# Kernel optimization log

Measured on AMD Instinct MI355X. Metric: run time of the kernel, lower is better.

## Reference

```python
import jax, jax.numpy as jnp
import numpy as np

EPS = 1e-12


def _l2norm(v):
    return v / (jnp.linalg.norm(v) + EPS)


def _sn(W, u):
    """One-step power-iteration spectral normalization (torch spectral_norm, 1x1 conv weight).
    W: (out, in), u: (out,). u/v are treated as buffers (no grad)."""
    Wm = W.reshape(W.shape[0], -1)
    v = _l2norm(Wm.T @ u)
    u2 = _l2norm(Wm @ v)
    u2 = jax.lax.stop_gradient(u2)
    v = jax.lax.stop_gradient(v)
    sigma = u2 @ (Wm @ v)
    return W / sigma


def _maxpool2(x):
    # 2x2 max pool, stride 2, NCHW
    N, C, H, W = x.shape
    return x.reshape(N, C, H // 2, 2, W // 2, 2).max(axis=(3, 5))


def setup_inputs() -> dict:
    key = jax.random.key(0)
    ks = jax.random.split(key, 10)
    N, C, H, W = 16, 256, 64, 64
    s = 0.05  # keep logits moderate
    return {
        "x": jax.random.normal(ks[0], (N, C, H, W), dtype=jnp.float32),
        "Wt": jax.random.normal(ks[1], (C >> 3, C), dtype=jnp.float32) * s,
        "Wp": jax.random.normal(ks[2], (C >> 3, C), dtype=jnp.float32) * s,
        "Wg": jax.random.normal(ks[3], (C >> 1, C), dtype=jnp.float32) * s,
        "Wo": jax.random.normal(ks[4], (C, C >> 1), dtype=jnp.float32) * s,
        "ut": jax.random.normal(ks[5], (C >> 3,), dtype=jnp.float32),
        "up": jax.random.normal(ks[6], (C >> 3,), dtype=jnp.float32),
        "ug": jax.random.normal(ks[7], (C >> 1,), dtype=jnp.float32),
        "uo": jax.random.normal(ks[8], (C,), dtype=jnp.float32),
        "gamma": jnp.float32(0.1),  # nonzero so attention branch is exercised
    }


def reference(x, Wt, Wp, Wg, Wo, ut, up, ug, uo, gamma):
    N, C, H, W = x.shape
    L = H * W          # location_num
    Ld = L // 4        # downsampled_num
    # 1x1 convs as channel einsums with spectrally-normalized weights
    theta = jnp.einsum('oc,nchw->nohw', _sn(Wt, ut), x).reshape(N, C >> 3, L)
    phi = _maxpool2(jnp.einsum('oc,nchw->nohw', _sn(Wp, up), x)).reshape(N, C >> 3, Ld)
    attn = jax.nn.softmax(jnp.einsum('ncl,ncm->nlm', theta, phi), axis=-1)  # (N, L, Ld)
    g = _maxpool2(jnp.einsum('oc,nchw->nohw', _sn(Wg, ug), x)).reshape(N, C >> 1, Ld)
    attn_g = jnp.einsum('ncm,nlm->ncl', g, attn).reshape(N, C >> 1, H, W)
    attn_g = jnp.einsum('oc,nchw->nohw', _sn(Wo, uo), attn_g)
    return x + gamma * attn_g
```

## Files before the change

kernel.cpp:

```cpp
#include <hip/hip_runtime.h>
#include <math.h>

#define EPS 1e-12f

typedef unsigned short ushort_t;
typedef __attribute__((ext_vector_type(8))) short short8;
typedef __attribute__((ext_vector_type(4))) float f32x4;
typedef __attribute__((ext_vector_type(4))) unsigned short ushort4v;
typedef __attribute__((ext_vector_type(2))) unsigned int uint2v;
typedef __attribute__((ext_vector_type(4))) unsigned int uint32x4;

#define WS_WB_F 0
#define WS_WO_F 24576
#define WS_TH_F 40960
#define WS_PH_F 1089536
#define WS_G_F  1351680

__device__ __forceinline__ ushort_t f2bf(float f) {
  unsigned int u = __float_as_uint(f);
  u += 0x7fffu + ((u >> 16) & 1u);
  return (ushort_t)(u >> 16);
}
__device__ __forceinline__ float bf2f(ushort_t u) {
  return __uint_as_float(((unsigned int)u) << 16);
}
__device__ __forceinline__ unsigned int pack_bfrh(float lo, float hi) {
  unsigned int a = __float_as_uint(lo) + 0x8000u;
  unsigned int b = __float_as_uint(hi) + 0x8000u;
  return (a >> 16) | (b & 0xffff0000u);
}
__device__ __forceinline__ float exp2_hw(float x) {
  float r;
  asm("v_exp_f32 %0, %1" : "=v"(r) : "v"(x));
  return r;
}

__device__ __forceinline__ void gload_lds16(const ushort_t* g, ushort_t* l) {
  __builtin_amdgcn_global_load_lds(
      (const __attribute__((address_space(1))) unsigned int*)g,
      (__attribute__((address_space(3))) unsigned int*)l, 16, 0, 0);
}

__device__ __forceinline__ float block_reduce_sum(float v, float* red) {
  int t = threadIdx.x;
  red[t] = v;
  __syncthreads();
  #pragma unroll
  for (int s = 128; s > 0; s >>= 1) {
    if (t < s) red[t] += red[t + s];
    __syncthreads();
  }
  float r = red[0];
  __syncthreads();
  return r;
}

__global__ __launch_bounds__(256) void sn_kernel(
    const float* __restrict__ Wt, const float* __restrict__ Wp,
    const float* __restrict__ Wg, const float* __restrict__ Wo,
    const float* __restrict__ ut, const float* __restrict__ up,
    const float* __restrict__ ug, const float* __restrict__ uo,
    float* __restrict__ ws) {
  __shared__ float red[256];
  __shared__ float ub[256];
  __shared__ float vb[256];
  const float* W; const float* u; int O, Ci;
  switch (blockIdx.x) {
    case 0:  W = Wt; u = ut; O = 32;  Ci = 256; break;
    case 1:  W = Wp; u = up; O = 32;  Ci = 256; break;
    case 2:  W = Wg; u = ug; O = 128; Ci = 256; break;
    default: W = Wo; u = uo; O = 256; Ci = 128; break;
  }
  int t = threadIdx.x;
  if (t < O) ub[t] = u[t];
  __syncthreads();
  float tv = 0.f;
  if (t < Ci) {
    for (int o = 0; o < O; o++) tv += W[o * Ci + t] * ub[o];
  }
  float nt2 = block_reduce_sum((t < Ci) ? tv * tv : 0.f, red);
  float ntn = sqrtf(nt2);
  if (t < Ci) vb[t] = tv / (ntn + EPS);
  __syncthreads();
  float sv = 0.f;
  if (t < O) {
    const float* Wr = W + (size_t)t * Ci;
    for (int c = 0; c < Ci; c += 4) {
      float4 wv = *(const float4*)(Wr + c);
      sv += wv.x * vb[c] + wv.y * vb[c + 1] + wv.z * vb[c + 2] + wv.w * vb[c + 3];
    }
  }
  float ss = block_reduce_sum((t < O) ? sv * sv : 0.f, red);
  float ns = sqrtf(ss);
  float sigma = ss / (ns + EPS);
  float inv = 1.f / sigma;
  if (blockIdx.x == 0) inv *= 1.44269504088896f;
  int total = O * Ci;
  if (blockIdx.x == 3) {
    ushort_t* dst = (ushort_t*)(ws + WS_WO_F);
    for (int i = t; i < total; i += 256) {
      int o = i >> 7, c = i & 127;
      int oct = o >> 4, l16o = o & 15, kc = c >> 5, cl = c & 31;
      int kap = (cl < 16) ? ((cl >> 2) * 8 + (cl & 3))
                          : (((cl >> 2) & 3) * 8 + 4 + (cl & 3));
      dst[(((kc * 16 + oct) * 64 + (kap >> 3) * 16 + l16o) << 3) + (kap & 7)] =
          f2bf(W[i] * inv);
    }
  } else {
    int base_row = (blockIdx.x == 0) ? 0 : (blockIdx.x == 1 ? 32 : 64);
    ushort_t* dst = (ushort_t*)(ws + WS_WB_F);
    for (int i = t; i < total; i += 256) {
      int o = i >> 8, c = i & 255;
      int og = base_row + o;
      int mtg = og >> 4, l16o = og & 15, kc = c >> 5, qd = (c >> 3) & 3, j = c & 7;
      dst[(((mtg * 8 + kc) * 64 + qd * 16 + l16o) << 3) + j] = f2bf(W[i] * inv);
    }
  }
}

__global__ __launch_bounds__(256, 2) void proj_mfma(
    const float* __restrict__ x, const ushort_t* __restrict__ wb,
    ushort_t* __restrict__ theta_b, ushort_t* __restrict__ phi_b,
    ushort_t* __restrict__ g_fb) {
  __shared__ ushort_t xb[128 * 264];
  const int t = threadIdx.x;
  const int n = blockIdx.y;
  const int l0 = blockIdx.x * 128;
  const float* xn = x + ((size_t)n * 256) * 4096 + l0;
  {
    const int lrel = t & 127;
    const int half = t >> 7;
    #pragma unroll 4
    for (int ch = 0; ch < 16; ++ch) {
      int chunk = half * 16 + ch;
      short8 v;
      #pragma unroll
      for (int j = 0; j < 8; ++j) {
        float f = xn[(size_t)(chunk * 8 + j) * 4096 + lrel];
        v[j] = (short)f2bf(f);
      }
      *(short8*)(&xb[lrel * 264 + chunk * 8]) = v;
    }
  }
  __syncthreads();
  const int w = t >> 6;
  const int lane = t & 63;
  const int quad = lane >> 4;
  const int l16 = lane & 15;
  const int rowA = (w * 16 + l16) * 264;
  const int rowB = (64 + w * 16 + l16) * 264;
  const int hd = blockIdx.x;
  #pragma unroll 1
  for (int pass = 0; pass < 2; ++pass) {
    f32x4 accA[6], accB[6];
    #pragma unroll
    for (int i = 0; i < 6; ++i) {
      accA[i] = (f32x4){0.f, 0.f, 0.f, 0.f};
      accB[i] = (f32x4){0.f, 0.f, 0.f, 0.f};
    }
    #pragma unroll
    for (int kc = 0; kc < 8; ++kc) {
      short8 bA = *(const short8*)(&xb[rowA + kc * 32 + quad * 8]);
      short8 bB = *(const short8*)(&xb[rowB + kc * 32 + quad * 8]);
      #pragma unroll
      for (int mt = 0; mt < 6; ++mt) {
        int mtg = pass * 6 + mt;
        short8 aW = *(const short8*)(wb + (((size_t)(mtg * 8 + kc) * 64 + lane) << 3));
        accA[mt] = __builtin_amdgcn_mfma_f32_16x16x32_bf16(aW, bA, accA[mt], 0, 0, 0);
        accB[mt] = __builtin_amdgcn_mfma_f32_16x16x32_bf16(aW, bB, accB[mt], 0, 0, 0);
      }
    }
    #pragma unroll
    for (int mt = 0; mt < 6; ++mt) {
      int mtg = pass * 6 + mt;
      if (mtg < 2) {
        int lA = l0 + w * 16 + l16;
        ushort4v vA, vB;
        #pragma unroll
        for (int r = 0; r < 4; ++r) { vA[r] = f2bf(accA[mt][r]); vB[r] = f2bf(accB[mt][r]); }
        *(ushort4v*)(theta_b + ((size_t)n * 4096 + lA) * 32 + mtg * 16 + quad * 4) = vA;
        *(ushort4v*)(theta_b + ((size_t)n * 4096 + lA + 64) * 32 + mtg * 16 + quad * 4) = vB;
      } else {
        float pm[4];
        #pragma unroll
        for (int r = 0; r < 4; ++r) {
          float v = fmaxf(accA[mt][r], accB[mt][r]);
          v = fmaxf(v, __shfl_xor(v, 1));
          pm[r] = v;
        }
        if ((l16 & 1) == 0) {
          int rr = l16 >> 1;
          if (mtg < 4) {
            int mp = hd * 32 + ((rr & 4) ? 16 : 0) + w * 4 + (rr & 3);
            ushort4v vv;
            #pragma unroll
            for (int r = 0; r < 4; ++r) vv[r] = f2bf(pm[r]);
            *(ushort4v*)(phi_b + ((size_t)n * 1024 + mp) * 32 + (mtg - 2) * 16 + quad * 4) = vv;
          } else {
            size_t fb = (size_t)n * 131072 +
                        (size_t)((hd * 8 + (mtg - 4)) * 64 + w * 16 + quad * 4) * 8 + rr;
            #pragma unroll
            for (int r = 0; r < 4; ++r)
              g_fb[fb + (size_t)r * 8] = f2bf(pm[r]);
          }
        }
      }
    }
  }
}

__global__ __launch_bounds__(256, 4) void attn_mfma(
    const float* __restrict__ x,
    const ushort_t* __restrict__ theta_b,
    const ushort_t* __restrict__ phi_b,
    const ushort_t* __restrict__ g_fb,
    const ushort_t* __restrict__ Wo_fb,
    const float* __restrict__ gamma_p,
    float* __restrict__ out) {
  __shared__ __align__(16) unsigned char smem[34816];
  ushort_t* gbuf = (ushort_t*)smem;
  ushort_t* outb = (ushort_t*)smem;

  const int t = threadIdx.x;
  const int w = t >> 6;
  const int lane = t & 63;
  const int quad = lane >> 4;
  const int l16 = lane & 15;

  const int flat = blockIdx.y * 64 + blockIdx.x;
  const int nf = ((flat & 7) << 7) | (flat >> 3);
  const int n = nf >> 6;
  const int l0 = (nf & 63) << 6;
  const int lq = l0 + w * 16;

  const short8 bth = *(const short8*)(theta_b + ((size_t)n * 4096 + lq + l16) * 32 + quad * 8);
  const ushort_t* phiN = phi_b + (size_t)n * 1024 * 32;
  const ushort_t* gN   = g_fb + (size_t)n * 131072;

  f32x4 oacc[8];
  #pragma unroll
  for (int j = 0; j < 8; ++j) oacc[j] = (f32x4){0.f, 0.f, 0.f, 0.f};
  float M = -3.0e38f, L = 0.f;
  unsigned int pk[16];

  auto STAGE = [&](int mc) {
    const ushort_t* src = gN + (size_t)mc * 16384 + w * 8 * 512 + lane * 8;
    ushort_t* dst = gbuf + w * 8 * 512;
    #pragma unroll
    for (int b = 0; b < 8; ++b)
      gload_lds16(src + b * 512, dst + b * 512);
  };

  auto QKSM = [&](int mc) {
    const int m0 = mc * 128;
    const f32x4 z = (f32x4){0.f, 0.f, 0.f, 0.f};
    f32x4 st[8];
    #pragma unroll
    for (int i = 0; i < 8; ++i) {
      short8 aph = *(const short8*)(phiN + (size_t)(m0 + i * 16 + l16) * 32 + quad * 8);
      st[i] = __builtin_amdgcn_mfma_f32_16x16x32_bf16(aph, bth, z, 0, 0, 0);
    }
    f32x4 a0 = st[0], a1 = st[1], a2 = st[2], a3 = st[3];
    #pragma unroll
    for (int r = 0; r < 4; ++r) {
      a0[r] = fmaxf(a0[r], st[4][r]); a1[r] = fmaxf(a1[r], st[5][r]);
      a2[r] = fmaxf(a2[r], st[6][r]); a3[r] = fmaxf(a3[r], st[7][r]);
    }
    #pragma unroll
    for (int r = 0; r < 4; ++r) { a0[r] = fmaxf(a0[r], a2[r]); a1[r] = fmaxf(a1[r], a3[r]); }
    float mlane = fmaxf(fmaxf(fmaxf(a0[0], a1[0]), fmaxf(a0[1], a1[1])),
                        fmaxf(fmaxf(a0[2], a1[2]), fmaxf(a0[3], a1[3])));
    if (!__all(mlane <= M + 8.0f)) {
      float mx = fmaxf(mlane, __shfl_xor(mlane, 16));
      mx = fmaxf(mx, __shfl_xor(mx, 32));
      float nm = fmaxf(M, mx);
      float al = exp2_hw(M - nm);
      M = nm;
      L *= al;
      #pragma unroll
      for (int j = 0; j < 8; ++j) {
        #pragma unroll
        for (int r = 0; r < 4; ++r) oacc[j][r] *= al;
      }
    }
    #pragma unroll
    for (int i = 0; i < 8; ++i) {
      #pragma unroll
      for (int r = 0; r < 4; ++r) st[i][r] = exp2_hw(st[i][r] - M);
    }
    f32x4 s0 = st[0], s1 = st[1];
    #pragma unroll
    for (int r = 0; r < 4; ++r) {
      s0[r] += st[2][r] + st[4][r] + st[6][r];
      s1[r] += st[3][r] + st[5][r] + st[7][r];
    }
    L += (s0[0] + s1[0]) + (s0[1] + s1[1]) + (s0[2] + s1[2]) + (s0[3] + s1[3]);
    #pragma unroll
    for (int i = 0; i < 8; ++i) {
      pk[2 * i]     = pack_bfrh(st[i][0], st[i][1]);
      pk[2 * i + 1] = pack_bfrh(st[i][2], st[i][3]);
    }
  };

  auto PV = [&]() {
    __builtin_amdgcn_s_setprio(1);
    #pragma unroll
    for (int s = 0; s < 4; ++s) {
      uint32x4 u = {pk[4 * s], pk[4 * s + 1], pk[4 * s + 2], pk[4 * s + 3]};
      short8 pb = __builtin_bit_cast(short8, u);
      #pragma unroll
      for (int j = 0; j < 8; ++j) {
        short8 gf = *(const short8*)(gbuf + (size_t)(s * 8 + j) * 512 + lane * 8);
        oacc[j] = __builtin_amdgcn_mfma_f32_16x16x32_bf16(gf, pb, oacc[j], 0, 0, 0);
      }
    }
    __builtin_amdgcn_s_setprio(0);
  };

  STAGE(0);
  QKSM(0);
  __syncthreads();
  #pragma unroll 1
  for (int mc = 0; mc < 8; ++mc) {
    PV();
    if (mc < 7) {
      __syncthreads();
      STAGE(mc + 1);
      QKSM(mc + 1);
      __syncthreads();
    }
  }
  __syncthreads();

  L += __shfl_xor(L, 16);
  L += __shfl_xor(L, 32);
  const float invL = 1.f / L;

  f32x4 acc2[16];
  #pragma unroll
  for (int i = 0; i < 16; ++i) acc2[i] = (f32x4){0.f, 0.f, 0.f, 0.f};

  short8 aO0, aO1, aO2, aO3;
  {
    uint32x4 u;
    u[0] = pack_bfrh(oacc[0][0] * invL, oacc[0][1] * invL);
    u[1] = pack_bfrh(oacc[0][2] * invL, oacc[0][3] * invL);
    u[2] = pack_bfrh(oacc[1][0] * invL, oacc[1][1] * invL);
    u[3] = pack_bfrh(oacc[1][2] * invL, oacc[1][3] * invL);
    aO0 = __builtin_bit_cast(short8, u);
    u[0] = pack_bfrh(oacc[2][0] * invL, oacc[2][1] * invL);
    u[1] = pack_bfrh(oacc[2][2] * invL, oacc[2][3] * invL);
    u[2] = pack_bfrh(oacc[3][0] * invL, oacc[3][1] * invL);
    u[3] = pack_bfrh(oacc[3][2] * invL, oacc[3][3] * invL);
    aO1 = __builtin_bit_cast(short8, u);
    u[0] = pack_bfrh(oacc[4][0] * invL, oacc[4][1] * invL);
    u[1] = pack_bfrh(oacc[4][2] * invL, oacc[4][3] * invL);
    u[2] = pack_bfrh(oacc[5][0] * invL, oacc[5][1] * invL);
    u[3] = pack_bfrh(oacc[5][2] * invL, oacc[5][3] * invL);
    aO2 = __builtin_bit_cast(short8, u);
    u[0] = pack_bfrh(oacc[6][0] * invL, oacc[6][1] * invL);
    u[1] = pack_bfrh(oacc[6][2] * invL, oacc[6][3] * invL);
    u[2] = pack_bfrh(oacc[7][0] * invL, oacc[7][1] * invL);
    u[3] = pack_bfrh(oacc[7][2] * invL, oacc[7][3] * invL);
    aO3 = __builtin_bit_cast(short8, u);
  }

  {
    const ushort_t* src = Wo_fb + w * 8 * 512 + lane * 8;
    ushort_t* dst = gbuf + w * 8 * 512;
    #pragma unroll
    for (int b = 0; b < 8; ++b)
      gload_lds16(src + b * 512, dst + b * 512);
  }
  __syncthreads();
  #pragma unroll
  for (int oct = 0; oct < 16; ++oct) {
    short8 bw0 = *(const short8*)(gbuf + (size_t)oct * 512 + lane * 8);
    short8 bw1 = *(const short8*)(gbuf + (size_t)(16 + oct) * 512 + lane * 8);
    acc2[oct] = __builtin_amdgcn_mfma_f32_16x16x32_bf16(aO0, bw0, acc2[oct], 0, 0, 0);
    acc2[oct] = __builtin_amdgcn_mfma_f32_16x16x32_bf16(aO1, bw1, acc2[oct], 0, 0, 0);
  }
  __syncthreads();
  {
    const ushort_t* src = Wo_fb + 16384 + w * 8 * 512 + lane * 8;
    ushort_t* dst = gbuf + w * 8 * 512;
    #pragma unroll
    for (int b = 0; b < 8; ++b)
      gload_lds16(src + b * 512, dst + b * 512);
  }
  __syncthreads();
  #pragma unroll
  for (int oct = 0; oct < 16; ++oct) {
    short8 bw2 = *(const short8*)(gbuf + (size_t)oct * 512 + lane * 8);
    short8 bw3 = *(const short8*)(gbuf + (size_t)(16 + oct) * 512 + lane * 8);
    acc2[oct] = __builtin_amdgcn_mfma_f32_16x16x32_bf16(aO2, bw2, acc2[oct], 0, 0, 0);
    acc2[oct] = __builtin_amdgcn_mfma_f32_16x16x32_bf16(aO3, bw3, acc2[oct], 0, 0, 0);
  }
  __syncthreads();
  #pragma unroll
  for (int oct = 0; oct < 16; ++oct) {
    uint2v p2;
    p2[0] = pack_bfrh(acc2[oct][0], acc2[oct][1]);
    p2[1] = pack_bfrh(acc2[oct][2], acc2[oct][3]);
    *(uint2v*)(&outb[(oct * 16 + l16) * 68 + w * 16 + quad * 4]) = p2;
  }
  __syncthreads();
  {
    const float gm = gamma_p[0];
    const int oc = (t >> 4);
    const int lch = (t & 15) * 4;
    #pragma unroll
    for (int ocg = 0; ocg < 16; ++ocg) {
      int row = ocg * 16 + oc;
      ushort4v ov = *(const ushort4v*)(&outb[row * 68 + lch]);
      const float* xp = x + ((size_t)n * 256 + row) * 4096 + l0 + lch;
      float* op = out + ((size_t)n * 256 + row) * 4096 + l0 + lch;
      float4 xv = *(const float4*)xp;
      float4 v;
      v.x = xv.x + gm * bf2f(ov[0]);
      v.y = xv.y + gm * bf2f(ov[1]);
      v.z = xv.z + gm * bf2f(ov[2]);
      v.w = xv.w + gm * bf2f(ov[3]);
      *(float4*)op = v;
    }
  }
}

extern "C" void kernel_launch(void* const* d_in, const int* in_sizes, int n_in,
                              void* d_out, int out_size, void* d_ws, size_t ws_size,
                              hipStream_t stream) {
  const float* x  = (const float*)d_in[0];
  const float* Wt = (const float*)d_in[1];
  const float* Wp = (const float*)d_in[2];
  const float* Wg = (const float*)d_in[3];
  const float* Wo = (const float*)d_in[4];
  const float* ut = (const float*)d_in[5];
  const float* up = (const float*)d_in[6];
  const float* ug = (const float*)d_in[7];
  const float* uo = (const float*)d_in[8];
  const float* gamma = (const float*)d_in[9];
  float* ws  = (float*)d_ws;
  float* out = (float*)d_out;

  ushort_t* wb      = (ushort_t*)(ws + WS_WB_F);
  ushort_t* Wo_b    = (ushort_t*)(ws + WS_WO_F);
  ushort_t* theta_b = (ushort_t*)(ws + WS_TH_F);
  ushort_t* phi_b   = (ushort_t*)(ws + WS_PH_F);
  ushort_t* g_fb    = (ushort_t*)(ws + WS_G_F);

  sn_kernel<<<4, 256, 0, stream>>>(Wt, Wp, Wg, Wo, ut, up, ug, uo, ws);
  proj_mfma<<<dim3(32, 16), 256, 0, stream>>>(x, wb, theta_b, phi_b, g_fb);
  attn_mfma<<<dim3(64, 16), 256, 0, stream>>>(x, theta_b, phi_b, g_fb, Wo_b, gamma, out);
}
```

Measured before the change: 201.0 us.

## Double-buffer g tiles in LDS and prefetch phi fragments across smaller chunks

Splits the key/value loop into 16 chunks of 64 positions instead of 8 of 128 and alternates between two 16KB LDS buffers. The next chunk's g tile is staged asynchronously while the current chunk runs QK, softmax and PV, and the next phi fragments are loaded into registers ahead of use. This is meant to hide global-to-LDS latency and cut the loop to one barrier per iteration instead of two. The cost is twice as many online-softmax max/rescale checks and smaller MFMA batches per iteration.

```diff
diff --git a/kernel.cpp b/kernel.cpp
--- a/kernel.cpp
+++ b/kernel.cpp
@@ -218,6 +218,8 @@
     const float* __restrict__ gamma_p,
     float* __restrict__ out) {
   __shared__ __align__(16) unsigned char smem[34816];
+  ushort_t* gb0  = (ushort_t*)smem;
+  ushort_t* gb1  = (ushort_t*)(smem + 16384);
   ushort_t* gbuf = (ushort_t*)smem;
   ushort_t* outb = (ushort_t*)smem;
 
@@ -241,33 +243,35 @@
   #pragma unroll
   for (int j = 0; j < 8; ++j) oacc[j] = (f32x4){0.f, 0.f, 0.f, 0.f};
   float M = -3.0e38f, L = 0.f;
-  unsigned int pk[16];
-
-  auto STAGE = [&](int mc) {
-    const ushort_t* src = gN + (size_t)mc * 16384 + w * 8 * 512 + lane * 8;
-    ushort_t* dst = gbuf + w * 8 * 512;
-    #pragma unroll
-    for (int b = 0; b < 8; ++b)
+  unsigned int pk[8];
+  short8 aph[4];
+
+  auto PRE = [&](int mc) {
+    #pragma unroll
+    for (int i = 0; i < 4; ++i)
+      aph[i] = *(const short8*)(phiN + (size_t)(mc * 64 + i * 16 + l16) * 32 + quad * 8);
+  };
+
+  auto STAGE = [&](int mc, ushort_t* buf) {
+    const ushort_t* src = gN + (size_t)mc * 8192 + w * 4 * 512 + lane * 8;
+    ushort_t* dst = buf + w * 4 * 512;
+    #pragma unroll
+    for (int b = 0; b < 4; ++b)
       gload_lds16(src + b * 512, dst + b * 512);
   };
 
-  auto QKSM = [&](int mc) {
-    const int m0 = mc * 128;
+  auto QKSM = [&]() {
     const f32x4 z = (f32x4){0.f, 0.f, 0.f, 0.f};
-    f32x4 st[8];
-    #pragma unroll
-    for (int i = 0; i < 8; ++i) {
-      short8 aph = *(const short8*)(phiN + (size_t)(m0 + i * 16 + l16) * 32 + quad * 8);
-      st[i] = __builtin_amdgcn_mfma_f32_16x16x32_bf16(aph, bth, z, 0, 0, 0);
-    }
-    f32x4 a0 = st[0], a1 = st[1], a2 = st[2], a3 = st[3];
+    f32x4 st[4];
+    #pragma unroll
+    for (int i = 0; i < 4; ++i)
+      st[i] = __builtin_amdgcn_mfma_f32_16x16x32_bf16(aph[i], bth, z, 0, 0, 0);
+    f32x4 a0 = st[0], a1 = st[1];
     #pragma unroll
     for (int r = 0; r < 4; ++r) {
-      a0[r] = fmaxf(a0[r], st[4][r]); a1[r] = fmaxf(a1[r], st[5][r]);
-      a2[r] = fmaxf(a2[r], st[6][r]); a3[r] = fmaxf(a3[r], st[7][r]);
-    }
-    #pragma unroll
-    for (int r = 0; r < 4; ++r) { a0[r] = fmaxf(a0[r], a2[r]); a1[r] = fmaxf(a1[r], a3[r]); }
+      a0[r] = fmaxf(a0[r], st[2][r]);
+      a1[r] = fmaxf(a1[r], st[3][r]);
+    }
     float mlane = fmaxf(fmaxf(fmaxf(a0[0], a1[0]), fmaxf(a0[1], a1[1])),
                         fmaxf(fmaxf(a0[2], a1[2]), fmaxf(a0[3], a1[3])));
     if (!__all(mlane <= M + 8.0f)) {
@@ -284,53 +288,49 @@
       }
     }
     #pragma unroll
-    for (int i = 0; i < 8; ++i) {
+    for (int i = 0; i < 4; ++i) {
       #pragma unroll
       for (int r = 0; r < 4; ++r) st[i][r] = exp2_hw(st[i][r] - M);
     }
-    f32x4 s0 = st[0], s1 = st[1];
-    #pragma unroll
-    for (int r = 0; r < 4; ++r) {
-      s0[r] += st[2][r] + st[4][r] + st[6][r];
-      s1[r] += st[3][r] + st[5][r] + st[7][r];
-    }
-    L += (s0[0] + s1[0]) + (s0[1] + s1[1]) + (s0[2] + s1[2]) + (s0[3] + s1[3]);
-    #pragma unroll
-    for (int i = 0; i < 8; ++i) {
+    f32x4 s0 = st[0];
+    #pragma unroll
+    for (int r = 0; r < 4; ++r) s0[r] += st[1][r] + st[2][r] + st[3][r];
+    L += (s0[0] + s0[1]) + (s0[2] + s0[3]);
+    #pragma unroll
+    for (int i = 0; i < 4; ++i) {
       pk[2 * i]     = pack_bfrh(st[i][0], st[i][1]);
       pk[2 * i + 1] = pack_bfrh(st[i][2], st[i][3]);
     }
   };
 
-  auto PV = [&]() {
+  auto PV = [&](ushort_t* buf) {
     __builtin_amdgcn_s_setprio(1);
     #pragma unroll
-    for (int s = 0; s < 4; ++s) {
+    for (int s = 0; s < 2; ++s) {
       uint32x4 u = {pk[4 * s], pk[4 * s + 1], pk[4 * s + 2], pk[4 * s + 3]};
       short8 pb = __builtin_bit_cast(short8, u);
       #pragma unroll
       for (int j = 0; j < 8; ++j) {
-        short8 gf = *(const short8*)(gbuf + (size_t)(s * 8 + j) * 512 + lane * 8);
+        short8 gf = *(const short8*)(buf + (size_t)(s * 8 + j) * 512 + lane * 8);
         oacc[j] = __builtin_amdgcn_mfma_f32_16x16x32_bf16(gf, pb, oacc[j], 0, 0, 0);
       }
     }
     __builtin_amdgcn_s_setprio(0);
   };
 
-  STAGE(0);
-  QKSM(0);
+  PRE(0);
+  STAGE(0, gb0);
   __syncthreads();
   #pragma unroll 1
-  for (int mc = 0; mc < 8; ++mc) {
-    PV();
-    if (mc < 7) {
-      __syncthreads();
-      STAGE(mc + 1);
-      QKSM(mc + 1);
-      __syncthreads();
-    }
-  }
-  __syncthreads();
+  for (int mc = 0; mc < 16; ++mc) {
+    ushort_t* cur = (mc & 1) ? gb1 : gb0;
+    ushort_t* nxt = (mc & 1) ? gb0 : gb1;
+    if (mc < 15) STAGE(mc + 1, nxt);
+    QKSM();
+    PV(cur);
+    if (mc < 15) PRE(mc + 1);
+    __syncthreads();
+  }
 
   L += __shfl_xor(L, 16);
   L += __shfl_xor(L, 32);
```

After: 203.5 us. Within noise of the previous version (+1.2%).
